# Kernel optimization log

Hardware: AMD Instinct MI355X
Metric: run time of the kernel (lower is better)

## Reference

```python
import jax, jax.numpy as jnp
import numpy as np

POS_MARGIN = 0.1
NEG_MARGIN = 1.4
LOG_SCALE = 24.0
MAX_POINTS = 256

N_FULL = 50000
M_C = 2048
N_C = 2048
D_FEAT = 256
K_CORR = 4096
N_BACK = 30000


def setup_inputs() -> dict:
    key = jax.random.key(0)
    ks = jax.random.split(key, 12)
    ref_feats = jax.random.normal(ks[4], (M_C, D_FEAT), jnp.float32)
    src_feats = jax.random.normal(ks[5], (N_C, D_FEAT), jnp.float32)
    # features are assumed L2-normalized (pairwise_distance(..., normalized=True))
    ref_feats = ref_feats / jnp.linalg.norm(ref_feats, axis=-1, keepdims=True)
    src_feats = src_feats / jnp.linalg.norm(src_feats, axis=-1, keepdims=True)
    return {
        "ref_points": jax.random.normal(ks[0], (N_FULL, 3), jnp.float32),
        "src_points": jax.random.normal(ks[1], (N_FULL, 3), jnp.float32),
        "ref_points_c": jax.random.normal(ks[2], (M_C, 3), jnp.float32),
        "src_points_c": jax.random.normal(ks[3], (N_C, 3), jnp.float32),
        "ref_feats_c": ref_feats,
        "src_feats_c": src_feats,
        "gt_node_corr_indices": jax.random.randint(ks[6], (K_CORR, 2), 0, M_C, dtype=jnp.int64) if jax.config.jax_enable_x64 else jax.random.randint(ks[6], (K_CORR, 2), 0, M_C, dtype=jnp.int32),
        "gt_node_corr_overlaps": jax.random.uniform(ks[7], (K_CORR,), jnp.float32),
        "corr_sp_mask": jax.random.uniform(ks[8], (M_C + N_C,), jnp.float32),
        "ref_back_indices": jax.random.randint(ks[9], (N_BACK,), 0, N_FULL, dtype=jnp.int32),
        "src_back_indices": jax.random.randint(ks[10], (N_BACK,), 0, N_FULL, dtype=jnp.int32),
    }


def _nn_indices(full_points, corr_points):
    # argmin over squared euclidean distance == argmin over cdist(p=2)
    d = (jnp.sum(corr_points ** 2, axis=1)[:, None]
         + jnp.sum(full_points ** 2, axis=1)[None, :]
         - 2.0 * corr_points @ full_points.T)  # [k, N]
    return jnp.argmin(d, axis=1)


def _forward(ref_points, src_points, ref_points_c, src_points_c,
             ref_feats_c, src_feats_c, gt_node_corr_overlaps, corr_sp_mask,
             gt_node_corr_indices, ref_back_indices, src_back_indices):
    m = ref_feats_c.shape[0]
    n = src_feats_c.shape[0]

    idx_ref = _nn_indices(ref_points, ref_points_c)  # [m]
    idx_src = _nn_indices(src_points, src_points_c)  # [n]

    # mask_ref[i] True iff idx_ref[i] appears in ref_back_indices (set intersection semantics)
    mask_ref = jnp.any(idx_ref[:, None] == ref_back_indices[None, :], axis=1)
    mask_src = jnp.any(idx_src[:, None] == src_back_indices[None, :], axis=1)

    xi = gt_node_corr_indices[:, 0]
    yi = gt_node_corr_indices[:, 1]
    corr_gt = jnp.zeros((m, n), dtype=bool).at[xi, yi].set(True)
    corr_overlap = jnp.zeros((m, n), jnp.float32).at[xi, yi].set(gt_node_corr_overlaps)

    corr_gt = corr_gt & (mask_ref[:, None] & mask_src[None, :])
    gt_mask = jnp.concatenate([mask_ref, mask_src]).astype(jnp.float32)  # [m+n]

    # cap number of positives at MAX_POINTS by overlap score
    count = jnp.sum(corr_gt)
    score = jnp.where(corr_gt, corr_overlap, -1.0).reshape(-1)
    topv, topi = jax.lax.top_k(score, MAX_POINTS)
    capped = jnp.zeros((m * n,), dtype=bool).at[topi].set(topv > -0.5).reshape(m, n)
    corr_gt = jnp.where(count > MAX_POINTS, capped, corr_gt)

    var_mask = 1.0 - corr_sp_mask  # [m+n]

    # NLLLaplace
    feat_sq = jnp.maximum(2.0 - 2.0 * (ref_feats_c @ src_feats_c.T), 0.0)
    feat_dists = jnp.sqrt(feat_sq)  # [m, n]
    laplace_mask = var_mask[:m][:, None] * var_mask[m:m + n][None, :]
    feat_dists = jnp.exp(0.5 * laplace_mask) * feat_dists

    not_pos = (~corr_gt).astype(jnp.float32)
    not_neg = corr_gt.astype(jnp.float32)
    pos_w = jax.lax.stop_gradient(
        jnp.maximum(feat_dists - 100000.0 * not_pos - POS_MARGIN, 0.0))
    neg_w = jax.lax.stop_gradient(
        jnp.maximum(NEG_MARGIN - (feat_dists + 100000.0 * not_neg), 0.0))

    lp = LOG_SCALE * (feat_dists - POS_MARGIN) * pos_w
    ln = LOG_SCALE * (NEG_MARGIN - feat_dists) * neg_w
    loss_row = jax.nn.softplus(jax.nn.logsumexp(lp, axis=-1) + jax.nn.logsumexp(ln, axis=-1)) / LOG_SCALE
    loss_col = jax.nn.softplus(jax.nn.logsumexp(lp, axis=-2) + jax.nn.logsumexp(ln, axis=-2)) / LOG_SCALE
    loss1 = (jnp.mean(loss_row) + jnp.mean(loss_col)) / 2.0
    loss2 = jnp.mean(jnp.abs(var_mask - gt_mask))
    loss = loss1 + loss2
    return loss, loss1, loss2


def reference(ref_points, src_points, ref_points_c, src_points_c,
              ref_feats_c, src_feats_c, gt_node_corr_indices,
              gt_node_corr_overlaps, corr_sp_mask,
              ref_back_indices, src_back_indices):
    return _forward(ref_points, src_points, ref_points_c, src_points_c,
                    ref_feats_c, src_feats_c, gt_node_corr_overlaps, corr_sp_mask,
                    gt_node_corr_indices, ref_back_indices, src_back_indices)
```

## Files before the change

kernel.cpp:

```cpp
#include <hip/hip_runtime.h>
#include <math.h>

using u8  = unsigned char;
using u32 = unsigned int;
using u64 = unsigned long long;

typedef short short8 __attribute__((ext_vector_type(8)));
typedef float f32x4  __attribute__((ext_vector_type(4)));
typedef float f32x2  __attribute__((ext_vector_type(2)));

#define MC 2048
#define NC 2048
#define DF 256
#define NFULL 50000
#define NBACK 30000
#define KCORR 4096
#define MAXPTS 256
#define NN_CHUNK 196
#define BM_WORDS_I 1568

constexpr size_t OFF_ROWP = 0;
constexpr size_t OFF_COLP = (size_t)2 * 1024 * 1024;
constexpr size_t OFF_GTB  = (size_t)3 * 1024 * 1024;
constexpr size_t OFF_NN   = OFF_GTB + (size_t)512 * 1024;
constexpr size_t OFF_CAND = OFF_NN + 4096 * 8;
constexpr size_t OFF_ACC  = OFF_CAND + 4096 * 8;
constexpr size_t OFF_CNT  = OFF_ACC + 256;
constexpr size_t OFF_BM   = OFF_CNT + 256;
constexpr size_t OFF_HASH = OFF_BM + 3200 * 4;

__device__ __forceinline__ u32 mask_of(const u64* nn, const u32* bm, int idx, int side) {
    u32 j = (u32)(nn[idx] & 0xFFFFFFFFull);
    return (bm[side * BM_WORDS_I + (j >> 5)] >> (j & 31)) & 1u;
}

__device__ __forceinline__ void circle_terms(float d, bool g, float& lp, float& ln) {
    if (g) { float a = d - 0.1f; lp = a > 0.f ? 24.f*a*a : 0.f; ln = 0.f; }
    else   { float b = 1.4f - d; ln = b > 0.f ? 24.f*b*b : 0.f; lp = 0.f; }
}

__device__ __forceinline__ float softplus_(float x) {
    return fmaxf(x, 0.f) + log1pf(expf(-fabsf(x)));
}

__device__ __forceinline__ void lse_merge(float& M, float& S, float M2, float S2) {
    float nm = fmaxf(M, M2);
    S = S * expf(M - nm) + S2 * expf(M2 - nm);
    M = nm;
}

__global__ __launch_bounds__(256) void k_init(uint4* __restrict__ gtb4, u64* __restrict__ nn,
                                              float* __restrict__ acc, u64* __restrict__ hash,
                                              u32* __restrict__ cnt, u32* __restrict__ bm) {
    int e = blockIdx.x * 256 + threadIdx.x;
    gtb4[e] = make_uint4(0u, 0u, 0u, 0u);
    if (e < 8192) hash[e] = 0ull;
    if (e < 4096) nn[e] = ~0ull;
    if (e < 2 * BM_WORDS_I) bm[e] = 0u;
    if (e < 8) acc[e] = 0.f;
    if (e < 8) cnt[e] = 0u;
}

__global__ __launch_bounds__(256) void k_nn(
        const float* __restrict__ fr, const float* __restrict__ fs,
        const float* __restrict__ cr, const float* __restrict__ cs,
        const int* __restrict__ rbi, const int* __restrict__ sbi,
        u32* __restrict__ bm, u64* __restrict__ nn) {
    const int side = blockIdx.y;
    const float* full = side ? fs : fr;
    const float* corr = side ? cs : cr;
    const int ib = blockIdx.x & 1, ch = blockIdx.x >> 1;
    const int t = threadIdx.x;

    int gb = side * 512 + blockIdx.x;
    if (gb < 235) {
        int e = gb * 256 + t;
        if (e < 2 * NBACK) {
            int s2 = e < NBACK ? 0 : 1;
            int v = s2 ? sbi[e - NBACK] : rbi[e];
            atomicOr(&bm[s2 * BM_WORDS_I + (v >> 5)], 1u << (v & 31));
        }
    }

    __shared__ float4 sx4[49], sy4[49], sz4[49], sw4[49];
    const int j0 = ch * NN_CHUNK;
    if (t < 49) {
        int b4 = j0 + t * 4;
        float xx[4], yy[4], zz[4], ww[4];
        #pragma unroll
        for (int u = 0; u < 4; ++u) {
            int j = b4 + u;
            if (j < NFULL) {
                float x = full[j*3], y = full[j*3+1], z = full[j*3+2];
                xx[u] = x; yy[u] = y; zz[u] = z;
                ww[u] = fmaf(x, x, fmaf(y, y, z*z));
            } else {
                xx[u] = 0.f; yy[u] = 0.f; zz[u] = 0.f; ww[u] = 3.0e38f;
            }
        }
        sx4[t] = make_float4(xx[0], xx[1], xx[2], xx[3]);
        sy4[t] = make_float4(yy[0], yy[1], yy[2], yy[3]);
        sz4[t] = make_float4(zz[0], zz[1], zz[2], zz[3]);
        sw4[t] = make_float4(ww[0], ww[1], ww[2], ww[3]);
    }

    float ax[4], ay[4], az[4], bd[4];
    int bg[4];
    #pragma unroll
    for (int q = 0; q < 4; ++q) {
        int i = ib * 1024 + q * 256 + t;
        float cx = corr[i*3], cy = corr[i*3+1], cz = corr[i*3+2];
        ax[q] = -2.f*cx; ay[q] = -2.f*cy; az[q] = -2.f*cz;
        bd[q] = 3.4e38f; bg[q] = 0;
    }
    __syncthreads();

    #pragma unroll 2
    for (int g = 0; g < 49; ++g) {
        float4 X = sx4[g], Y = sy4[g], Z = sz4[g], W = sw4[g];
        f32x2 xlo = {X.x, X.y}, xhi = {X.z, X.w};
        f32x2 ylo = {Y.x, Y.y}, yhi = {Y.z, Y.w};
        f32x2 zlo = {Z.x, Z.y}, zhi = {Z.z, Z.w};
        f32x2 wlo = {W.x, W.y}, whi = {W.z, W.w};
        #pragma unroll
        for (int q = 0; q < 4; ++q) {
            f32x2 aq = {ax[q], ax[q]}, bq = {ay[q], ay[q]}, cq2 = {az[q], az[q]};
            f32x2 dlo = __builtin_elementwise_fma(aq, xlo,
                          __builtin_elementwise_fma(bq, ylo,
                            __builtin_elementwise_fma(cq2, zlo, wlo)));
            f32x2 dhi = __builtin_elementwise_fma(aq, xhi,
                          __builtin_elementwise_fma(bq, yhi,
                            __builtin_elementwise_fma(cq2, zhi, whi)));
            f32x2 m2 = __builtin_elementwise_min(dlo, dhi);
            float gm = fminf(m2.x, m2.y);
            bool win = gm < bd[q];
            bd[q] = fminf(bd[q], gm);
            bg[q] = win ? g : bg[q];
        }
    }

    #pragma unroll
    for (int q = 0; q < 4; ++q) {
        int gsel = bg[q];
        float4 X = sx4[gsel], Y = sy4[gsel], Z = sz4[gsel], W = sw4[gsel];
        f32x2 xlo = {X.x, X.y}, xhi = {X.z, X.w};
        f32x2 ylo = {Y.x, Y.y}, yhi = {Y.z, Y.w};
        f32x2 zlo = {Z.x, Z.y}, zhi = {Z.z, Z.w};
        f32x2 wlo = {W.x, W.y}, whi = {W.z, W.w};
        f32x2 aq = {ax[q], ax[q]}, bq = {ay[q], ay[q]}, cq2 = {az[q], az[q]};
        f32x2 dlo = __builtin_elementwise_fma(aq, xlo,
                      __builtin_elementwise_fma(bq, ylo,
                        __builtin_elementwise_fma(cq2, zlo, wlo)));
        f32x2 dhi = __builtin_elementwise_fma(aq, xhi,
                      __builtin_elementwise_fma(bq, yhi,
                        __builtin_elementwise_fma(cq2, zhi, whi)));
        float dv[4] = {dlo.x, dlo.y, dhi.x, dhi.y};
        u32 bj = (u32)(j0 + gsel * 4);
        bool found = false;
        #pragma unroll
        for (int u = 0; u < 4; ++u) {
            if (!found && dv[u] == bd[q]) { bj = (u32)(j0 + gsel*4 + u); found = true; }
        }
        int i = ib * 1024 + q * 256 + t;
        float cn = 0.25f * fmaf(ax[q], ax[q], fmaf(ay[q], ay[q], az[q]*az[q]));
        float bf = bd[q] + cn;
        u32 db = __float_as_uint(bf);
        db = (db & 0x80000000u) ? ~db : (db | 0x80000000u);
        atomicMin(&nn[side * 2048 + i], ((u64)db << 32) | bj);
    }
}

__global__ __launch_bounds__(256) void k_msc(
        const u64* __restrict__ nn, const u32* __restrict__ bm,
        const float* __restrict__ spm, const int* __restrict__ gti,
        u32* __restrict__ gtb, u64* __restrict__ hash, float* __restrict__ acc) {
    const int t = threadIdx.x;
    if (blockIdx.x == 0) {
        __shared__ float red[4];
        float c = 0.f;
        for (int e = t; e < 4096; e += 256)
            c += fabsf((1.f - spm[e]) - (float)mask_of(nn, bm, e, e >> 11));
        for (int o = 32; o; o >>= 1) c += __shfl_xor(c, o);
        if ((t & 63) == 0) red[t >> 6] = c;
        __syncthreads();
        if (t == 0) acc[2] = red[0] + red[1] + red[2] + red[3];
    }

    int k = blockIdx.x * 256 + t;
    int xi = gti[2*k], yi = gti[2*k+1];
    u32 cell = (u32)(xi * 2048 + yi);
    u32 masked = mask_of(nn, bm, xi, 0) & mask_of(nn, bm, 2048 + yi, 1);
    if (masked) atomicOr(&gtb[xi * 64 + (yi >> 5)], 1u << (yi & 31));
    u64 val = ((u64)(cell + 1) << 13) | ((u64)masked << 12) | (u32)k;
    u32 h = (cell * 2654435761u) >> 19;
    while (true) {
        u64 cur = hash[h];
        if (cur == 0ull) cur = atomicCAS(&hash[h], 0ull, val);
        if (cur == 0ull) break;
        if ((cur >> 13) == (u64)(cell + 1)) { atomicMax(&hash[h], val); break; }
        h = (h + 1) & 8191;
    }
}

__global__ void k_scat2(const u64* __restrict__ hash, const float* __restrict__ gtv,
                        u64* __restrict__ cand, u32* __restrict__ cnt) {
    int e = blockIdx.x * 256 + threadIdx.x;
    u64 s = hash[e];
    if (s == 0ull) return;
    if (!((s >> 12) & 1ull)) return;
    u32 cell = (u32)(s >> 13) - 1u;
    u32 k = (u32)(s & 0xFFFull);
    u32 vb = __float_as_uint(gtv[k]);
    u32 idx = atomicAdd(cnt, 1u);
    cand[idx] = ((u64)vb << 22) | (u32)(0x3FFFFF - cell);
}

__global__ __launch_bounds__(256) void k_top(const u64* __restrict__ cand,
                                             const u32* __restrict__ cnt,
                                             u32* __restrict__ gtb) {
    const int n = (int)cnt[0];
    if (n <= MAXPTS) return;
    if (blockIdx.x * 256 >= n) return;
    __shared__ u64 keys[4096];
    const int t = threadIdx.x;
    for (int e = t; e < n; e += 256) keys[e] = cand[e];
    __syncthreads();
    int c = blockIdx.x * 256 + t;
    if (c >= n) return;
    u64 me = keys[c];
    int rank = 0;
    #pragma unroll 4
    for (int j = 0; j < n; ++j) rank += (keys[j] > me);
    if (rank >= MAXPTS) {
        u32 cell = 0x3FFFFFu - (u32)(me & 0x3FFFFFull);
        int row = cell >> 11, col = cell & 2047;
        atomicAnd(&gtb[row * 64 + (col >> 5)], ~(1u << (col & 31)));
    }
}

__global__ __launch_bounds__(256) void k_gemm(
        const float* __restrict__ A, const float* __restrict__ B,
        const float* __restrict__ spm, const u32* __restrict__ gtb,
        float4* __restrict__ rowp, float4* __restrict__ colp) {
    __shared__ __align__(16) short As[16384];
    __shared__ __align__(16) short Bs[8192];
    __shared__ u32 gtw[256];
    const int t = threadIdx.x;
    const int l = t & 63, wid = t >> 6;
    const int wm = wid >> 1, wn = wid & 1;
    const int i0 = blockIdx.y * 128, j0 = blockIdx.x * 64;

    gtw[t] = gtb[(size_t)(i0 + (t >> 1)) * 64 + (j0 >> 5) + (t & 1)];

    f32x4 acc[4][2] = {};

    for (int ks = 0; ks < 2; ++ks) {
        __syncthreads();
        #pragma unroll
        for (int it = 0; it < 12; ++it) {
            int sl = it * 256 + t;
            int c = sl & 63, q = c >> 4, r15 = c & 15;
            const float* src;
            short* dst;
            int kf;
            if (it < 8) {
                int frag = sl >> 6;
                kf = frag & 3;
                int row = (frag >> 2) * 16 + r15;
                src = A + (size_t)(i0 + row) * 256;
                dst = &As[sl * 8];
            } else {
                int sl2 = sl - 2048;
                int frag = sl2 >> 6;
                kf = frag & 3;
                int row = (frag >> 2) * 16 + r15;
                src = B + (size_t)(j0 + row) * 256;
                dst = &Bs[sl2 * 8];
            }
            int col = ks * 128 + kf * 32 + q * 8;
            float4 v0 = *(const float4*)(src + col);
            float4 v1 = *(const float4*)(src + col + 4);
            u32 w0 = __builtin_amdgcn_perm(__float_as_uint(v0.y), __float_as_uint(v0.x), 0x07060302u);
            u32 w1 = __builtin_amdgcn_perm(__float_as_uint(v0.w), __float_as_uint(v0.z), 0x07060302u);
            u32 w2 = __builtin_amdgcn_perm(__float_as_uint(v1.y), __float_as_uint(v1.x), 0x07060302u);
            u32 w3 = __builtin_amdgcn_perm(__float_as_uint(v1.w), __float_as_uint(v1.z), 0x07060302u);
            *(uint4*)dst = make_uint4(w0, w1, w2, w3);
        }
        __syncthreads();

        #pragma unroll
        for (int kf = 0; kf < 4; ++kf) {
            short8 a[4], b[2];
            #pragma unroll
            for (int mi = 0; mi < 4; ++mi)
                a[mi] = *(const short8*)&As[(((wm*4 + mi)*4 + kf) << 9) + l*8];
            #pragma unroll
            for (int ni = 0; ni < 2; ++ni)
                b[ni] = *(const short8*)&Bs[(((wn*2 + ni)*4 + kf) << 9) + l*8];
            #pragma unroll
            for (int mi = 0; mi < 4; ++mi)
                #pragma unroll
                for (int ni = 0; ni < 2; ++ni)
                    acc[mi][ni] = __builtin_amdgcn_mfma_f32_16x16x32_bf16(
                        a[mi], b[ni], acc[mi][ni], 0, 0, 0);
        }
    }

    const int cq = l >> 4, cr = l & 15;
    const int rows0 = i0 + wm * 64, cols0 = j0 + wn * 32;

    float vmj[2];
    #pragma unroll
    for (int ni = 0; ni < 2; ++ni) vmj[ni] = 1.f - spm[2048 + cols0 + ni*16 + cr];
    float vmi[4][4];
    #pragma unroll
    for (int mi = 0; mi < 4; ++mi)
        #pragma unroll
        for (int rr = 0; rr < 4; ++rr)
            vmi[mi][rr] = 1.f - spm[rows0 + mi*16 + cq*4 + rr];

    u32 gmask = 0;
    #pragma unroll
    for (int mi = 0; mi < 4; ++mi)
        #pragma unroll
        for (int rr = 0; rr < 4; ++rr) {
            u32 w = gtw[(wm*64 + mi*16 + cq*4 + rr) * 2 + wn];
            #pragma unroll
            for (int ni = 0; ni < 2; ++ni)
                if ((w >> (ni*16 + cr)) & 1u) gmask |= 1u << (mi*8 + ni*4 + rr);
        }
    #pragma unroll
    for (int mi = 0; mi < 4; ++mi)
        #pragma unroll
        for (int ni = 0; ni < 2; ++ni)
            #pragma unroll
            for (int rr = 0; rr < 4; ++rr) {
                float s  = acc[mi][ni][rr];
                float fs = fmaxf(2.f - 2.f*s, 0.f);
                acc[mi][ni][rr] = sqrtf(fs) * expf(0.5f * vmi[mi][rr] * vmj[ni]);
            }

    const int jt2 = blockIdx.x * 2 + wn;
    const int it2 = blockIdx.y * 2 + wm;

    #pragma unroll
    for (int mi = 0; mi < 4; ++mi)
        #pragma unroll
        for (int rr = 0; rr < 4; ++rr) {
            float lp0, ln0, lp1, ln1;
            circle_terms(acc[mi][0][rr], (gmask >> (mi*8 + rr)) & 1, lp0, ln0);
            circle_terms(acc[mi][1][rr], (gmask >> (mi*8 + 4 + rr)) & 1, lp1, ln1);
            float mp = fmaxf(lp0, lp1), mn = fmaxf(ln0, ln1);
            #pragma unroll
            for (int o = 1; o < 16; o <<= 1) {
                mp = fmaxf(mp, __shfl_xor(mp, o));
                mn = fmaxf(mn, __shfl_xor(mn, o));
            }
            float sp = expf(lp0 - mp) + expf(lp1 - mp);
            float sn = expf(ln0 - mn) + expf(ln1 - mn);
            #pragma unroll
            for (int o = 1; o < 16; o <<= 1) {
                sp += __shfl_xor(sp, o);
                sn += __shfl_xor(sn, o);
            }
            if (cr == mi*4 + rr) {
                int row = rows0 + mi*16 + cq*4 + rr;
                rowp[(size_t)jt2 * 2048 + row] = make_float4(mp, sp, mn, sn);
            }
        }

    #pragma unroll
    for (int ni = 0; ni < 2; ++ni) {
        float lp[16], ln[16];
        #pragma unroll
        for (int mi = 0; mi < 4; ++mi)
            #pragma unroll
            for (int rr = 0; rr < 4; ++rr)
                circle_terms(acc[mi][ni][rr], (gmask >> (mi*8 + ni*4 + rr)) & 1,
                             lp[mi*4+rr], ln[mi*4+rr]);
        float mp = lp[0], mn = ln[0];
        #pragma unroll
        for (int e = 1; e < 16; ++e) { mp = fmaxf(mp, lp[e]); mn = fmaxf(mn, ln[e]); }
        #pragma unroll
        for (int o = 16; o < 64; o <<= 1) {
            mp = fmaxf(mp, __shfl_xor(mp, o));
            mn = fmaxf(mn, __shfl_xor(mn, o));
        }
        float sp = 0.f, sn = 0.f;
        #pragma unroll
        for (int e = 0; e < 16; ++e) { sp += expf(lp[e] - mp); sn += expf(ln[e] - mn); }
        #pragma unroll
        for (int o = 16; o < 64; o <<= 1) {
            sp += __shfl_xor(sp, o);
            sn += __shfl_xor(sn, o);
        }
        if (cq == 0) {
            int col = cols0 + ni*16 + cr;
            colp[(size_t)it2 * 2048 + col] = make_float4(mp, sp, mn, sn);
        }
    }
}

__global__ __launch_bounds__(256) void k_merge(const float4* __restrict__ rowp,
                                               const float4* __restrict__ colp,
                                               float* __restrict__ acc,
                                               u32* __restrict__ cnt,
                                               float* __restrict__ out) {
    const int t = threadIdx.x;
    const int b = blockIdx.x;
    const int sub = t & 3;
    float Mp = -1e30f, Sp = 0.f, Mn = -1e30f, Sn = 0.f;

    if (b < 32) {
        int row = (b * 256 + t) >> 2;
        int base = sub * 16;
        #pragma unroll
        for (int j = 0; j < 16; j += 8) {
            float4 pb[8];
            #pragma unroll
            for (int u = 0; u < 8; ++u)
                pb[u] = rowp[(size_t)(base + j + u) * 2048 + row];
            #pragma unroll
            for (int u = 0; u < 8; ++u) {
                lse_merge(Mp, Sp, pb[u].x, pb[u].y);
                lse_merge(Mn, Sn, pb[u].z, pb[u].w);
            }
        }
    } else {
        int col = ((b - 32) * 256 + t) >> 2;
        int base = sub * 8;
        float4 pb[8];
        #pragma unroll
        for (int u = 0; u < 8; ++u)
            pb[u] = colp[(size_t)(base + u) * 2048 + col];
        #pragma unroll
        for (int u = 0; u < 8; ++u) {
            lse_merge(Mp, Sp, pb[u].x, pb[u].y);
            lse_merge(Mn, Sn, pb[u].z, pb[u].w);
        }
    }

    #pragma unroll
    for (int o = 1; o < 4; o <<= 1) {
        float M2 = __shfl_xor(Mp, o), S2 = __shfl_xor(Sp, o);
        lse_merge(Mp, Sp, M2, S2);
        M2 = __shfl_xor(Mn, o); S2 = __shfl_xor(Sn, o);
        lse_merge(Mn, Sn, M2, S2);
    }

    float lv = 0.f;
    if (sub == 0) {
        float x = (Mp + logf(Sp)) + (Mn + logf(Sn));
        lv = softplus_(x) * (1.f / 24.f);
    }
    for (int o = 32; o; o >>= 1) lv += __shfl_xor(lv, o);
    __shared__ float wsum[4];
    __shared__ u32 tic;
    if ((t & 63) == 0) wsum[t >> 6] = lv;
    __syncthreads();
    if (t == 0) {
        atomicAdd(&acc[b < 32 ? 0 : 1], wsum[0] + wsum[1] + wsum[2] + wsum[3]);
        __threadfence();
        tic = atomicAdd(&cnt[1], 1u);
    }
    __syncthreads();
    if (t == 0 && tic == 63u) {
        __threadfence();
        float a0 = atomicAdd(&acc[0], 0.f);
        float a1 = atomicAdd(&acc[1], 0.f);
        float a2 = atomicAdd(&acc[2], 0.f);
        float l1 = (a0 + a1) * (0.5f / 2048.f);
        float l2 = a2 * (1.f / 4096.f);
        out[0] = l1 + l2; out[1] = l1; out[2] = l2;
    }
}

extern "C" void kernel_launch(void* const* d_in, const int* in_sizes, int n_in,
                              void* d_out, int out_size, void* d_ws, size_t ws_size,
                              hipStream_t stream) {
    (void)in_sizes; (void)n_in; (void)out_size; (void)ws_size;
    const float* ref_points = (const float*)d_in[0];
    const float* src_points = (const float*)d_in[1];
    const float* ref_c      = (const float*)d_in[2];
    const float* src_c      = (const float*)d_in[3];
    const float* ref_f      = (const float*)d_in[4];
    const float* src_f      = (const float*)d_in[5];
    const int*   gti        = (const int*)d_in[6];
    const float* gtv        = (const float*)d_in[7];
    const float* spm        = (const float*)d_in[8];
    const int*   rbi        = (const int*)d_in[9];
    const int*   sbi        = (const int*)d_in[10];

    char* ws = (char*)d_ws;
    float4* rowp = (float4*)(ws + OFF_ROWP);
    float4* colp = (float4*)(ws + OFF_COLP);
    u32*   gtb  = (u32*)  (ws + OFF_GTB);
    u64*   nn   = (u64*)  (ws + OFF_NN);
    u64*   cand = (u64*)  (ws + OFF_CAND);
    float* acc  = (float*)(ws + OFF_ACC);
    u32*   cnt  = (u32*)  (ws + OFF_CNT);
    u32*   bm   = (u32*)  (ws + OFF_BM);
    u64*   hash = (u64*)  (ws + OFF_HASH);

    k_init <<<128, 256, 0, stream>>>((uint4*)gtb, nn, acc, hash, cnt, bm);
    k_nn   <<<dim3(512, 2), 256, 0, stream>>>(ref_points, src_points, ref_c, src_c,
                                              rbi, sbi, bm, nn);
    k_msc  <<<16, 256, 0, stream>>>(nn, bm, spm, gti, gtb, hash, acc);
    k_scat2<<<32, 256, 0, stream>>>(hash, gtv, cand, cnt);
    k_top  <<<16, 256, 0, stream>>>(cand, cnt, gtb);
    k_gemm <<<dim3(32, 16), 256, 0, stream>>>(ref_f, src_f, spm, gtb, rowp, colp);
    k_merge<<<64, 256, 0, stream>>>(rowp, colp, acc, cnt, (float*)d_out);
}
```

Measured before the change: 110.7 us.

## Fuse mask/scatter/top-k kernels with grid barriers and widen NN grid

Merges the mask/hash, candidate scatter and top-k pruning kernels into one 32-block kernel that uses global atomic-counter barriers between phases, cutting two kernel launches and their gaps. The NN kernel also processes 512 correspondence points per block instead of 1024, doubling the grid for more parallelism at the cost of more shared-memory chunk loads and atomics. The grid barrier relies on all 32 blocks being co-resident and on init zeroing the barrier counters.

Result: no change. 110.4 us (-0.4%).

```diff
diff --git a/kernel.cpp b/kernel.cpp
--- a/kernel.cpp
+++ b/kernel.cpp
@@ -29,6 +29,7 @@
 constexpr size_t OFF_BM   = OFF_CNT + 256;
 constexpr size_t OFF_HASH = OFF_BM + 3200 * 4;
 
+
 __device__ __forceinline__ u32 mask_of(const u64* nn, const u32* bm, int idx, int side) {
     u32 j = (u32)(nn[idx] & 0xFFFFFFFFull);
     return (bm[side * BM_WORDS_I + (j >> 5)] >> (j & 31)) & 1u;
@@ -47,6 +48,16 @@
     float nm = fmaxf(M, M2);
     S = S * expf(M - nm) + S2 * expf(M2 - nm);
     M = nm;
+}
+
+__device__ __forceinline__ void block_barrier(u32* counter, u32 target, u32* s_tic) {
+    __threadfence();
+    __syncthreads();
+    if (threadIdx.x == 0) {
+        *s_tic = atomicAdd(counter, 1u);
+        while (__hip_atomic_load(counter, __ATOMIC_ACQUIRE, __HIP_MEMORY_SCOPE_AGENT) < target) {}
+    }
+    __syncthreads();
 }
 
 __global__ __launch_bounds__(256) void k_init(uint4* __restrict__ gtb4, u64* __restrict__ nn,
@@ -69,10 +80,10 @@
     const int side = blockIdx.y;
     const float* full = side ? fs : fr;
     const float* corr = side ? cs : cr;
-    const int ib = blockIdx.x & 1, ch = blockIdx.x >> 1;
+    const int ib = blockIdx.x & 3, ch = blockIdx.x >> 2;
     const int t = threadIdx.x;
 
-    int gb = side * 512 + blockIdx.x;
+    int gb = side * 1024 + blockIdx.x;
     if (gb < 235) {
         int e = gb * 256 + t;
         if (e < 2 * NBACK) {
@@ -104,11 +115,11 @@
         sw4[t] = make_float4(ww[0], ww[1], ww[2], ww[3]);
     }
 
-    float ax[4], ay[4], az[4], bd[4];
-    int bg[4];
-    #pragma unroll
-    for (int q = 0; q < 4; ++q) {
-        int i = ib * 1024 + q * 256 + t;
+    float ax[2], ay[2], az[2], bd[2];
+    int bg[2];
+    #pragma unroll
+    for (int q = 0; q < 2; ++q) {
+        int i = ib * 512 + q * 256 + t;
         float cx = corr[i*3], cy = corr[i*3+1], cz = corr[i*3+2];
         ax[q] = -2.f*cx; ay[q] = -2.f*cy; az[q] = -2.f*cz;
         bd[q] = 3.4e38f; bg[q] = 0;
@@ -123,7 +134,7 @@
         f32x2 zlo = {Z.x, Z.y}, zhi = {Z.z, Z.w};
         f32x2 wlo = {W.x, W.y}, whi = {W.z, W.w};
         #pragma unroll
-        for (int q = 0; q < 4; ++q) {
+        for (int q = 0; q < 2; ++q) {
             f32x2 aq = {ax[q], ax[q]}, bq = {ay[q], ay[q]}, cq2 = {az[q], az[q]};
             f32x2 dlo = __builtin_elementwise_fma(aq, xlo,
                           __builtin_elementwise_fma(bq, ylo,
@@ -140,7 +151,7 @@
     }
 
     #pragma unroll
-    for (int q = 0; q < 4; ++q) {
+    for (int q = 0; q < 2; ++q) {
         int gsel = bg[q];
         float4 X = sx4[gsel], Y = sy4[gsel], Z = sz4[gsel], W = sw4[gsel];
         f32x2 xlo = {X.x, X.y}, xhi = {X.z, X.w};
@@ -161,7 +172,7 @@
         for (int u = 0; u < 4; ++u) {
             if (!found && dv[u] == bd[q]) { bj = (u32)(j0 + gsel*4 + u); found = true; }
         }
-        int i = ib * 1024 + q * 256 + t;
+        int i = ib * 512 + q * 256 + t;
         float cn = 0.25f * fmaf(ax[q], ax[q], fmaf(ay[q], ay[q], az[q]*az[q]));
         float bf = bd[q] + cn;
         u32 db = __float_as_uint(bf);
@@ -173,10 +184,30 @@
 __global__ __launch_bounds__(256) void k_msc(
         const u64* __restrict__ nn, const u32* __restrict__ bm,
         const float* __restrict__ spm, const int* __restrict__ gti,
-        u32* __restrict__ gtb, u64* __restrict__ hash, float* __restrict__ acc) {
-    const int t = threadIdx.x;
-    if (blockIdx.x == 0) {
-        __shared__ float red[4];
+        const float* __restrict__ gtv,
+        u32* __restrict__ gtb, u64* __restrict__ hash, u64* __restrict__ cand,
+        u32* __restrict__ cnt, float* __restrict__ acc) {
+    const int b = blockIdx.x, t = threadIdx.x;
+    __shared__ u64 keys[4096];
+    __shared__ u32 s_tic;
+
+    if (b < 16) {
+        int k = b * 256 + t;
+        int xi = gti[2*k], yi = gti[2*k+1];
+        u32 cell = (u32)(xi * 2048 + yi);
+        u32 masked = mask_of(nn, bm, xi, 0) & mask_of(nn, bm, 2048 + yi, 1);
+        if (masked) atomicOr(&gtb[xi * 64 + (yi >> 5)], 1u << (yi & 31));
+        u64 val = ((u64)(cell + 1) << 13) | ((u64)masked << 12) | (u32)k;
+        u32 h = (cell * 2654435761u) >> 19;
+        while (true) {
+            u64 cur = hash[h];
+            if (cur == 0ull) cur = atomicCAS(&hash[h], 0ull, val);
+            if (cur == 0ull) break;
+            if ((cur >> 13) == (u64)(cell + 1)) { atomicMax(&hash[h], val); break; }
+            h = (h + 1) & 8191;
+        }
+    } else if (b == 16) {
+        float* red = (float*)keys;
         float c = 0.f;
         for (int e = t; e < 4096; e += 256)
             c += fabsf((1.f - spm[e]) - (float)mask_of(nn, bm, e, e >> 11));
@@ -185,56 +216,40 @@
         __syncthreads();
         if (t == 0) acc[2] = red[0] + red[1] + red[2] + red[3];
     }
-
-    int k = blockIdx.x * 256 + t;
-    int xi = gti[2*k], yi = gti[2*k+1];
-    u32 cell = (u32)(xi * 2048 + yi);
-    u32 masked = mask_of(nn, bm, xi, 0) & mask_of(nn, bm, 2048 + yi, 1);
-    if (masked) atomicOr(&gtb[xi * 64 + (yi >> 5)], 1u << (yi & 31));
-    u64 val = ((u64)(cell + 1) << 13) | ((u64)masked << 12) | (u32)k;
-    u32 h = (cell * 2654435761u) >> 19;
-    while (true) {
-        u64 cur = hash[h];
-        if (cur == 0ull) cur = atomicCAS(&hash[h], 0ull, val);
-        if (cur == 0ull) break;
-        if ((cur >> 13) == (u64)(cell + 1)) { atomicMax(&hash[h], val); break; }
-        h = (h + 1) & 8191;
-    }
-}
-
-__global__ void k_scat2(const u64* __restrict__ hash, const float* __restrict__ gtv,
-                        u64* __restrict__ cand, u32* __restrict__ cnt) {
-    int e = blockIdx.x * 256 + threadIdx.x;
-    u64 s = hash[e];
-    if (s == 0ull) return;
-    if (!((s >> 12) & 1ull)) return;
-    u32 cell = (u32)(s >> 13) - 1u;
-    u32 k = (u32)(s & 0xFFFull);
-    u32 vb = __float_as_uint(gtv[k]);
-    u32 idx = atomicAdd(cnt, 1u);
-    cand[idx] = ((u64)vb << 22) | (u32)(0x3FFFFF - cell);
-}
-
-__global__ __launch_bounds__(256) void k_top(const u64* __restrict__ cand,
-                                             const u32* __restrict__ cnt,
-                                             u32* __restrict__ gtb) {
-    const int n = (int)cnt[0];
-    if (n <= MAXPTS) return;
-    if (blockIdx.x * 256 >= n) return;
-    __shared__ u64 keys[4096];
-    const int t = threadIdx.x;
-    for (int e = t; e < n; e += 256) keys[e] = cand[e];
-    __syncthreads();
-    int c = blockIdx.x * 256 + t;
-    if (c >= n) return;
-    u64 me = keys[c];
-    int rank = 0;
-    #pragma unroll 4
-    for (int j = 0; j < n; ++j) rank += (keys[j] > me);
-    if (rank >= MAXPTS) {
-        u32 cell = 0x3FFFFFu - (u32)(me & 0x3FFFFFull);
-        int row = cell >> 11, col = cell & 2047;
-        atomicAnd(&gtb[row * 64 + (col >> 5)], ~(1u << (col & 31)));
+    block_barrier(&cnt[2], 32u, &s_tic);
+
+    {
+        int e = b * 256 + t;
+        u64 s = __hip_atomic_load(&hash[e], __ATOMIC_RELAXED, __HIP_MEMORY_SCOPE_AGENT);
+        if (s != 0ull && ((s >> 12) & 1ull)) {
+            u32 cell = (u32)(s >> 13) - 1u;
+            u32 kk = (u32)(s & 0xFFFull);
+            u32 vb = __float_as_uint(gtv[kk]);
+            u32 idx = atomicAdd(&cnt[0], 1u);
+            cand[idx] = ((u64)vb << 22) | (u32)(0x3FFFFF - cell);
+        }
+    }
+    block_barrier(&cnt[3], 32u, &s_tic);
+
+    if (b < 16) {
+        const int n = (int)__hip_atomic_load(&cnt[0], __ATOMIC_RELAXED, __HIP_MEMORY_SCOPE_AGENT);
+        if (n > MAXPTS && b * 256 < n) {
+            for (int e = t; e < n; e += 256)
+                keys[e] = __hip_atomic_load(&cand[e], __ATOMIC_RELAXED, __HIP_MEMORY_SCOPE_AGENT);
+            __syncthreads();
+            int c = b * 256 + t;
+            if (c < n) {
+                u64 me = keys[c];
+                int rank = 0;
+                #pragma unroll 4
+                for (int j = 0; j < n; ++j) rank += (keys[j] > me);
+                if (rank >= MAXPTS) {
+                    u32 cell = 0x3FFFFFu - (u32)(me & 0x3FFFFFull);
+                    int row = cell >> 11, col = cell & 2047;
+                    atomicAnd(&gtb[row * 64 + (col >> 5)], ~(1u << (col & 31)));
+                }
+            }
+        }
     }
 }
 
@@ -503,11 +518,9 @@
     u64*   hash = (u64*)  (ws + OFF_HASH);
 
     k_init <<<128, 256, 0, stream>>>((uint4*)gtb, nn, acc, hash, cnt, bm);
-    k_nn   <<<dim3(512, 2), 256, 0, stream>>>(ref_points, src_points, ref_c, src_c,
-                                              rbi, sbi, bm, nn);
-    k_msc  <<<16, 256, 0, stream>>>(nn, bm, spm, gti, gtb, hash, acc);
-    k_scat2<<<32, 256, 0, stream>>>(hash, gtv, cand, cnt);
-    k_top  <<<16, 256, 0, stream>>>(cand, cnt, gtb);
+    k_nn   <<<dim3(1024, 2), 256, 0, stream>>>(ref_points, src_points, ref_c, src_c,
+                                               rbi, sbi, bm, nn);
+    k_msc  <<<32, 256, 0, stream>>>(nn, bm, spm, gti, gtv, gtb, hash, cand, cnt, acc);
     k_gemm <<<dim3(32, 16), 256, 0, stream>>>(ref_f, src_f, spm, gtb, rowp, colp);
     k_merge<<<64, 256, 0, stream>>>(rowp, colp, acc, cnt, (float*)d_out);
 }
```
